# Kernel optimization log

Measured on AMD Instinct MI355X. Metric: run time of the kernel, lower is better.

## Reference

```python
import jax, jax.numpy as jnp
import numpy as np

N_CELLS = 4096          # rows of sparse x
N_INPUT_GENES = 20000   # cols of sparse x == len(input_gene_list)
N_PRETRAINED = 30000    # rows of embedding table
NUM_HID = 128
NNZ = 2097152           # ~512 expressed genes per cell


def setup_inputs() -> dict:
    key = jax.random.key(0)
    k_val, k_row, k_col, k_gidx, k_emb = jax.random.split(key, 5)
    x_values = jax.random.uniform(k_val, (NNZ,), dtype=jnp.float32)
    x_rows = jnp.sort(jax.random.randint(k_row, (NNZ,), 0, N_CELLS))
    x_cols = jax.random.randint(k_col, (NNZ,), 0, N_INPUT_GENES)
    gene_idx = jax.random.randint(k_gidx, (N_INPUT_GENES,), 0, N_PRETRAINED)
    # nn.Parameter(torch.randn(...) * 0.005)
    embs = jax.random.normal(k_emb, (N_PRETRAINED, NUM_HID), dtype=jnp.float32) * 0.005
    return {"x_values": x_values, "x_rows": x_rows, "x_cols": x_cols,
            "gene_idx": gene_idx, "embs": embs}


def reference(x_values, x_rows, x_cols, gene_idx, embs):
    # feat = F.embedding(gene_idx, embs)           -> [G_in, H]
    # out  = torch.sparse.mm(x, feat)              -> [N_cells, H]
    # Fused: gather per-nnz embedding rows, scale by value, segment-sum by cell.
    feat = embs[gene_idx]                                   # [G_in, H]
    contrib = x_values[:, None] * feat[x_cols]              # [NNZ, H]
    out = jax.ops.segment_sum(contrib, x_rows,
                              num_segments=N_CELLS,
                              indices_are_sorted=True)      # [N_cells, H]
    return out
```

## Files before the change

kernel.cpp:

```cpp
#include <hip/hip_runtime.h>

#define NNZ_TOT    2097152
#define N_CELLS    4096
#define N_GIN      20000
#define N_PRE      30000
#define NUM_HID    128

#define GA_OFF    0
#define GA_BYTES  ((size_t)NNZ_TOT * 4)
#define EBF_OFF   (GA_OFF + GA_BYTES)
#define EBF_BYTES ((size_t)N_PRE * NUM_HID * 2)
#define RP_OFF    (EBF_OFF + EBF_BYTES)
#define RP_BYTES  ((((size_t)(N_CELLS + 1) * 4) + 255) & ~(size_t)255)
#define WS_NEED   (RP_OFF + RP_BYTES)

__device__ __forceinline__ unsigned short f2bf(float f) {
    union { float f; unsigned u; } c; c.f = f;
    unsigned u = c.u;
    u += 0x7fffu + ((u >> 16) & 1u);
    return (unsigned short)(u >> 16);
}

#define NB_GA ((NNZ_TOT + 255) / 256)
#define NB_RP ((N_CELLS + 256) / 256)

__global__ __launch_bounds__(256) void precompute_kernel(
    const int* __restrict__ xc, const int* __restrict__ gidx,
    const int* __restrict__ xr, int* __restrict__ g_arr,
    int* __restrict__ rp)
{
    const int b = blockIdx.x;
    if (b < NB_GA) {
        const int i = b * 256 + threadIdx.x;
        if (i < NNZ_TOT) g_arr[i] = gidx[xc[i]];
    } else {
        const int r = (b - NB_GA) * 256 + threadIdx.x;
        if (r <= N_CELLS) {
            int lo = 0, hi = NNZ_TOT;
            while (lo < hi) {
                const int mid = (lo + hi) >> 1;
                if (xr[mid] < r) lo = mid + 1; else hi = mid;
            }
            rp[r] = lo;
        }
    }
}

__global__ __launch_bounds__(256) void convert_embs_kernel(
    const float* __restrict__ embs, unsigned short* __restrict__ ebf)
{
    const int i = blockIdx.x * blockDim.x + threadIdx.x;
    if (i * 4 < N_PRE * NUM_HID) {
        const float4 f = *reinterpret_cast<const float4*>(&embs[i * 4]);
        ushort4 o;
        o.x = f2bf(f.x); o.y = f2bf(f.y); o.z = f2bf(f.z); o.w = f2bf(f.w);
        *reinterpret_cast<ushort4*>(&ebf[i * 4]) = o;
    }
}

__device__ __forceinline__ void fma8(uint4 f, float vv, float4& a0, float4& a1) {
    a0.x = fmaf(vv, __uint_as_float(f.x << 16),         a0.x);
    a0.y = fmaf(vv, __uint_as_float(f.x & 0xffff0000u), a0.y);
    a0.z = fmaf(vv, __uint_as_float(f.y << 16),         a0.z);
    a0.w = fmaf(vv, __uint_as_float(f.y & 0xffff0000u), a0.w);
    a1.x = fmaf(vv, __uint_as_float(f.z << 16),         a1.x);
    a1.y = fmaf(vv, __uint_as_float(f.z & 0xffff0000u), a1.y);
    a1.z = fmaf(vv, __uint_as_float(f.w << 16),         a1.z);
    a1.w = fmaf(vv, __uint_as_float(f.w & 0xffff0000u), a1.w);
}

__global__ __launch_bounds__(256) void omics_row_kernel(
    const float*          __restrict__ xv,
    const int*            __restrict__ ga,
    const int*            __restrict__ rp,
    const unsigned short* __restrict__ ebf,
    float*                __restrict__ out)
{
    const int wave = (blockIdx.x * blockDim.x + threadIdx.x) >> 6;
    const int lane = threadIdx.x & 63;
    const int sub  = lane & 15;
    const int quad = lane >> 4;
    const int r    = __builtin_amdgcn_readfirstlane(wave);
    if (r >= N_CELLS) return;

    const int lo = rp[r];
    const int hi = rp[r + 1];
    const int h8 = sub * 8;

    float4 a0 = make_float4(0.f, 0.f, 0.f, 0.f);
    float4 a1 = make_float4(0.f, 0.f, 0.f, 0.f);
    float4 b0 = make_float4(0.f, 0.f, 0.f, 0.f);
    float4 b1 = make_float4(0.f, 0.f, 0.f, 0.f);

    int i = lo;
    for (; i + 32 <= hi; i += 32) {
        const int i0 = i + quad;
        const int g0 = ga[i0];      const float v0 = xv[i0];
        const int g1 = ga[i0 + 4];  const float v1 = xv[i0 + 4];
        const int g2 = ga[i0 + 8];  const float v2 = xv[i0 + 8];
        const int g3 = ga[i0 + 12]; const float v3 = xv[i0 + 12];
        const int g4 = ga[i0 + 16]; const float v4 = xv[i0 + 16];
        const int g5 = ga[i0 + 20]; const float v5 = xv[i0 + 20];
        const int g6 = ga[i0 + 24]; const float v6 = xv[i0 + 24];
        const int g7 = ga[i0 + 28]; const float v7 = xv[i0 + 28];

        const uint4 f0 = *reinterpret_cast<const uint4*>(&ebf[(long)g0 * NUM_HID + h8]);
        const uint4 f1 = *reinterpret_cast<const uint4*>(&ebf[(long)g1 * NUM_HID + h8]);
        const uint4 f2 = *reinterpret_cast<const uint4*>(&ebf[(long)g2 * NUM_HID + h8]);
        const uint4 f3 = *reinterpret_cast<const uint4*>(&ebf[(long)g3 * NUM_HID + h8]);
        const uint4 f4 = *reinterpret_cast<const uint4*>(&ebf[(long)g4 * NUM_HID + h8]);
        const uint4 f5 = *reinterpret_cast<const uint4*>(&ebf[(long)g5 * NUM_HID + h8]);
        const uint4 f6 = *reinterpret_cast<const uint4*>(&ebf[(long)g6 * NUM_HID + h8]);
        const uint4 f7 = *reinterpret_cast<const uint4*>(&ebf[(long)g7 * NUM_HID + h8]);

        fma8(f0, v0, a0, a1);
        fma8(f1, v1, b0, b1);
        fma8(f2, v2, a0, a1);
        fma8(f3, v3, b0, b1);
        fma8(f4, v4, a0, a1);
        fma8(f5, v5, b0, b1);
        fma8(f6, v6, a0, a1);
        fma8(f7, v7, b0, b1);
    }
    for (; i < hi; i += 4) {
        const int  idx = i + quad;
        const bool ok  = idx < hi;
        const int   gg = ga[ok ? idx : (hi - 1)];
        const float vv = ok ? xv[idx] : 0.f;
        const uint4 f  = *reinterpret_cast<const uint4*>(&ebf[(long)gg * NUM_HID + h8]);
        fma8(f, vv, a0, a1);
    }

    a0.x += b0.x; a0.y += b0.y; a0.z += b0.z; a0.w += b0.w;
    a1.x += b1.x; a1.y += b1.y; a1.z += b1.z; a1.w += b1.w;

    a0.x += __shfl_xor(a0.x, 16); a0.x += __shfl_xor(a0.x, 32);
    a0.y += __shfl_xor(a0.y, 16); a0.y += __shfl_xor(a0.y, 32);
    a0.z += __shfl_xor(a0.z, 16); a0.z += __shfl_xor(a0.z, 32);
    a0.w += __shfl_xor(a0.w, 16); a0.w += __shfl_xor(a0.w, 32);
    a1.x += __shfl_xor(a1.x, 16); a1.x += __shfl_xor(a1.x, 32);
    a1.y += __shfl_xor(a1.y, 16); a1.y += __shfl_xor(a1.y, 32);
    a1.z += __shfl_xor(a1.z, 16); a1.z += __shfl_xor(a1.z, 32);
    a1.w += __shfl_xor(a1.w, 16); a1.w += __shfl_xor(a1.w, 32);

    if (quad == 0) {
        float* o = &out[(long)r * NUM_HID + h8];
        *reinterpret_cast<float4*>(o)     = a0;
        *reinterpret_cast<float4*>(o + 4) = a1;
    }
}

__global__ __launch_bounds__(256) void omics_fp32_row_kernel(
    const float* __restrict__ xv, const int* __restrict__ xr,
    const int* __restrict__ xc, const int* __restrict__ gidx,
    const float* __restrict__ embs, float* __restrict__ out)
{
    const int wave = (blockIdx.x * blockDim.x + threadIdx.x) >> 6;
    const int lane = threadIdx.x & 63;
    if (wave >= N_CELLS) return;
    int lo = 0, hi = NNZ_TOT;
    while (lo < hi) { int m = (lo + hi) >> 1; if (xr[m] < wave) lo = m + 1; else hi = m; }
    int lo2 = lo, hi2 = NNZ_TOT;
    while (lo2 < hi2) { int m = (lo2 + hi2) >> 1; if (xr[m] < wave + 1) lo2 = m + 1; else hi2 = m; }
    const int h = lane * 2;
    float2 acc = make_float2(0.f, 0.f);
    for (int i = lo; i < lo2; ++i) {
        const float v = xv[i];
        const int   g = gidx[xc[i]];
        const float2 f = *reinterpret_cast<const float2*>(&embs[(long)g * NUM_HID + h]);
        acc.x = fmaf(v, f.x, acc.x);
        acc.y = fmaf(v, f.y, acc.y);
    }
    *reinterpret_cast<float2*>(&out[(long)wave * NUM_HID + h]) = acc;
}

extern "C" void kernel_launch(void* const* d_in, const int* in_sizes, int n_in,
                              void* d_out, int out_size, void* d_ws, size_t ws_size,
                              hipStream_t stream) {
    const float* xv   = (const float*)d_in[0];
    const int*   xr   = (const int*)  d_in[1];
    const int*   xc   = (const int*)  d_in[2];
    const int*   gidx = (const int*)  d_in[3];
    const float* embs = (const float*)d_in[4];
    float*       out  = (float*)d_out;

    if (ws_size >= WS_NEED) {
        int*            ga  = (int*)((char*)d_ws + GA_OFF);
        unsigned short* ebf = (unsigned short*)((char*)d_ws + EBF_OFF);
        int*            rp  = (int*)((char*)d_ws + RP_OFF);

        precompute_kernel<<<NB_GA + NB_RP, 256, 0, stream>>>(xc, gidx, xr, ga, rp);
        convert_embs_kernel<<<(N_PRE * NUM_HID / 4 + 255) / 256, 256, 0, stream>>>(embs, ebf);

        omics_row_kernel<<<(N_CELLS * 64) / 256, 256, 0, stream>>>(
            xv, ga, rp, ebf, out);
    } else {
        omics_fp32_row_kernel<<<(N_CELLS * 64) / 256, 256, 0, stream>>>(
            xv, xr, xc, gidx, embs, out);
    }
}
```

Baseline: 135.3 us.

## Split embedding table into column halves mapped to separate XCD groups

The bf16 embedding table is stored as two column halves, and each half of the output columns is computed by blocks whose index maps them to one group of four XCDs. The intent is to shrink the per-XCD L2 working set of gathered embedding rows so it fits in cache better. In exchange, each row's index and value streams are read twice, once per half, and those reads now use nontemporal loads and stores. The speedup depends on the round-robin block-to-XCD placement holding.

```diff
diff --git a/kernel.cpp b/kernel.cpp
--- a/kernel.cpp
+++ b/kernel.cpp
@@ -5,14 +5,18 @@
 #define N_GIN      20000
 #define N_PRE      30000
 #define NUM_HID    128
-
-#define GA_OFF    0
-#define GA_BYTES  ((size_t)NNZ_TOT * 4)
-#define EBF_OFF   (GA_OFF + GA_BYTES)
-#define EBF_BYTES ((size_t)N_PRE * NUM_HID * 2)
-#define RP_OFF    (EBF_OFF + EBF_BYTES)
-#define RP_BYTES  ((((size_t)(N_CELLS + 1) * 4) + 255) & ~(size_t)255)
-#define WS_NEED   (RP_OFF + RP_BYTES)
+#define HID_HALF   64
+
+#define GA_OFF     0
+#define GA_BYTES   ((size_t)NNZ_TOT * 4)
+#define EBFH_BYTES ((size_t)N_PRE * HID_HALF * 2)
+#define EBF0_OFF   (GA_OFF + GA_BYTES)
+#define EBF1_OFF   (EBF0_OFF + EBFH_BYTES)
+#define RP_OFF     (EBF1_OFF + EBFH_BYTES)
+#define RP_BYTES   ((((size_t)(N_CELLS + 1) * 4) + 255) & ~(size_t)255)
+#define WS_NEED    (RP_OFF + RP_BYTES)
+
+typedef float vfloat4 __attribute__((ext_vector_type(4)));
 
 __device__ __forceinline__ unsigned short f2bf(float f) {
     union { float f; unsigned u; } c; c.f = f;
@@ -47,14 +51,19 @@
 }
 
 __global__ __launch_bounds__(256) void convert_embs_kernel(
-    const float* __restrict__ embs, unsigned short* __restrict__ ebf)
+    const float* __restrict__ embs, unsigned short* __restrict__ ebf0,
+    unsigned short* __restrict__ ebf1)
 {
     const int i = blockIdx.x * blockDim.x + threadIdx.x;
-    if (i * 4 < N_PRE * NUM_HID) {
-        const float4 f = *reinterpret_cast<const float4*>(&embs[i * 4]);
+    const long idx = (long)i * 4;
+    if (idx < (long)N_PRE * NUM_HID) {
+        const float4 f = *reinterpret_cast<const float4*>(&embs[idx]);
         ushort4 o;
         o.x = f2bf(f.x); o.y = f2bf(f.y); o.z = f2bf(f.z); o.w = f2bf(f.w);
-        *reinterpret_cast<ushort4*>(&ebf[i * 4]) = o;
+        const int row = (int)(idx >> 7);
+        const int col = (int)(idx & 127);
+        unsigned short* __restrict__ dst = (col < HID_HALF) ? ebf0 : ebf1;
+        *reinterpret_cast<ushort4*>(&dst[row * HID_HALF + (col & 63)]) = o;
     }
 }
 
@@ -69,19 +78,25 @@
     a1.w = fmaf(vv, __uint_as_float(f.w & 0xffff0000u), a1.w);
 }
 
-__global__ __launch_bounds__(256) void omics_row_kernel(
+__global__ __launch_bounds__(256) void omics_half_kernel(
     const float*          __restrict__ xv,
     const int*            __restrict__ ga,
     const int*            __restrict__ rp,
-    const unsigned short* __restrict__ ebf,
+    const unsigned short* __restrict__ ebf0,
+    const unsigned short* __restrict__ ebf1,
     float*                __restrict__ out)
 {
-    const int wave = (blockIdx.x * blockDim.x + threadIdx.x) >> 6;
+    const int blk  = blockIdx.x;
+    const int xcd  = blk & 7;
+    const int half = xcd >> 2;
+    const int grp  = ((blk >> 3) << 2) | (xcd & 3);
+    const int wid  = threadIdx.x >> 6;
     const int lane = threadIdx.x & 63;
-    const int sub  = lane & 15;
-    const int quad = lane >> 4;
-    const int r    = __builtin_amdgcn_readfirstlane(wave);
-    if (r >= N_CELLS) return;
+    const int sub  = lane & 7;
+    const int oct  = lane >> 3;
+    const int r    = __builtin_amdgcn_readfirstlane((grp << 2) | wid);
+
+    const unsigned short* __restrict__ eb = half ? ebf1 : ebf0;
 
     const int lo = rp[r];
     const int hi = rp[r + 1];
@@ -93,25 +108,33 @@
     float4 b1 = make_float4(0.f, 0.f, 0.f, 0.f);
 
     int i = lo;
-    for (; i + 32 <= hi; i += 32) {
-        const int i0 = i + quad;
-        const int g0 = ga[i0];      const float v0 = xv[i0];
-        const int g1 = ga[i0 + 4];  const float v1 = xv[i0 + 4];
-        const int g2 = ga[i0 + 8];  const float v2 = xv[i0 + 8];
-        const int g3 = ga[i0 + 12]; const float v3 = xv[i0 + 12];
-        const int g4 = ga[i0 + 16]; const float v4 = xv[i0 + 16];
-        const int g5 = ga[i0 + 20]; const float v5 = xv[i0 + 20];
-        const int g6 = ga[i0 + 24]; const float v6 = xv[i0 + 24];
-        const int g7 = ga[i0 + 28]; const float v7 = xv[i0 + 28];
-
-        const uint4 f0 = *reinterpret_cast<const uint4*>(&ebf[(long)g0 * NUM_HID + h8]);
-        const uint4 f1 = *reinterpret_cast<const uint4*>(&ebf[(long)g1 * NUM_HID + h8]);
-        const uint4 f2 = *reinterpret_cast<const uint4*>(&ebf[(long)g2 * NUM_HID + h8]);
-        const uint4 f3 = *reinterpret_cast<const uint4*>(&ebf[(long)g3 * NUM_HID + h8]);
-        const uint4 f4 = *reinterpret_cast<const uint4*>(&ebf[(long)g4 * NUM_HID + h8]);
-        const uint4 f5 = *reinterpret_cast<const uint4*>(&ebf[(long)g5 * NUM_HID + h8]);
-        const uint4 f6 = *reinterpret_cast<const uint4*>(&ebf[(long)g6 * NUM_HID + h8]);
-        const uint4 f7 = *reinterpret_cast<const uint4*>(&ebf[(long)g7 * NUM_HID + h8]);
+    for (; i + 64 <= hi; i += 64) {
+        const int i0 = i + oct;
+        const int g0 = __builtin_nontemporal_load(ga + i0);
+        const int g1 = __builtin_nontemporal_load(ga + i0 + 8);
+        const int g2 = __builtin_nontemporal_load(ga + i0 + 16);
+        const int g3 = __builtin_nontemporal_load(ga + i0 + 24);
+        const int g4 = __builtin_nontemporal_load(ga + i0 + 32);
+        const int g5 = __builtin_nontemporal_load(ga + i0 + 40);
+        const int g6 = __builtin_nontemporal_load(ga + i0 + 48);
+        const int g7 = __builtin_nontemporal_load(ga + i0 + 56);
+        const float v0 = __builtin_nontemporal_load(xv + i0);
+        const float v1 = __builtin_nontemporal_load(xv + i0 + 8);
+        const float v2 = __builtin_nontemporal_load(xv + i0 + 16);
+        const float v3 = __builtin_nontemporal_load(xv + i0 + 24);
+        const float v4 = __builtin_nontemporal_load(xv + i0 + 32);
+        const float v5 = __builtin_nontemporal_load(xv + i0 + 40);
+        const float v6 = __builtin_nontemporal_load(xv + i0 + 48);
+        const float v7 = __builtin_nontemporal_load(xv + i0 + 56);
+
+        const uint4 f0 = *reinterpret_cast<const uint4*>(&eb[(long)g0 * HID_HALF + h8]);
+        const uint4 f1 = *reinterpret_cast<const uint4*>(&eb[(long)g1 * HID_HALF + h8]);
+        const uint4 f2 = *reinterpret_cast<const uint4*>(&eb[(long)g2 * HID_HALF + h8]);
+        const uint4 f3 = *reinterpret_cast<const uint4*>(&eb[(long)g3 * HID_HALF + h8]);
+        const uint4 f4 = *reinterpret_cast<const uint4*>(&eb[(long)g4 * HID_HALF + h8]);
+        const uint4 f5 = *reinterpret_cast<const uint4*>(&eb[(long)g5 * HID_HALF + h8]);
+        const uint4 f6 = *reinterpret_cast<const uint4*>(&eb[(long)g6 * HID_HALF + h8]);
+        const uint4 f7 = *reinterpret_cast<const uint4*>(&eb[(long)g7 * HID_HALF + h8]);
 
         fma8(f0, v0, a0, a1);
         fma8(f1, v1, b0, b1);
@@ -122,31 +145,33 @@
         fma8(f6, v6, a0, a1);
         fma8(f7, v7, b0, b1);
     }
-    for (; i < hi; i += 4) {
-        const int  idx = i + quad;
+    for (; i < hi; i += 8) {
+        const int  idx = i + oct;
         const bool ok  = idx < hi;
-        const int   gg = ga[ok ? idx : (hi - 1)];
+        const int   gg = ga[ok ? idx : lo];
         const float vv = ok ? xv[idx] : 0.f;
-        const uint4 f  = *reinterpret_cast<const uint4*>(&ebf[(long)gg * NUM_HID + h8]);
+        const uint4 f  = *reinterpret_cast<const uint4*>(&eb[(long)gg * HID_HALF + h8]);
         fma8(f, vv, a0, a1);
     }
 
     a0.x += b0.x; a0.y += b0.y; a0.z += b0.z; a0.w += b0.w;
     a1.x += b1.x; a1.y += b1.y; a1.z += b1.z; a1.w += b1.w;
 
-    a0.x += __shfl_xor(a0.x, 16); a0.x += __shfl_xor(a0.x, 32);
-    a0.y += __shfl_xor(a0.y, 16); a0.y += __shfl_xor(a0.y, 32);
-    a0.z += __shfl_xor(a0.z, 16); a0.z += __shfl_xor(a0.z, 32);
-    a0.w += __shfl_xor(a0.w, 16); a0.w += __shfl_xor(a0.w, 32);
-    a1.x += __shfl_xor(a1.x, 16); a1.x += __shfl_xor(a1.x, 32);
-    a1.y += __shfl_xor(a1.y, 16); a1.y += __shfl_xor(a1.y, 32);
-    a1.z += __shfl_xor(a1.z, 16); a1.z += __shfl_xor(a1.z, 32);
-    a1.w += __shfl_xor(a1.w, 16); a1.w += __shfl_xor(a1.w, 32);
-
-    if (quad == 0) {
-        float* o = &out[(long)r * NUM_HID + h8];
-        *reinterpret_cast<float4*>(o)     = a0;
-        *reinterpret_cast<float4*>(o + 4) = a1;
+    a0.x += __shfl_xor(a0.x, 8); a0.x += __shfl_xor(a0.x, 16); a0.x += __shfl_xor(a0.x, 32);
+    a0.y += __shfl_xor(a0.y, 8); a0.y += __shfl_xor(a0.y, 16); a0.y += __shfl_xor(a0.y, 32);
+    a0.z += __shfl_xor(a0.z, 8); a0.z += __shfl_xor(a0.z, 16); a0.z += __shfl_xor(a0.z, 32);
+    a0.w += __shfl_xor(a0.w, 8); a0.w += __shfl_xor(a0.w, 16); a0.w += __shfl_xor(a0.w, 32);
+    a1.x += __shfl_xor(a1.x, 8); a1.x += __shfl_xor(a1.x, 16); a1.x += __shfl_xor(a1.x, 32);
+    a1.y += __shfl_xor(a1.y, 8); a1.y += __shfl_xor(a1.y, 16); a1.y += __shfl_xor(a1.y, 32);
+    a1.z += __shfl_xor(a1.z, 8); a1.z += __shfl_xor(a1.z, 16); a1.z += __shfl_xor(a1.z, 32);
+    a1.w += __shfl_xor(a1.w, 8); a1.w += __shfl_xor(a1.w, 16); a1.w += __shfl_xor(a1.w, 32);
+
+    if (oct == 0) {
+        float* o = &out[(long)r * NUM_HID + half * HID_HALF + h8];
+        const vfloat4 s0 = { a0.x, a0.y, a0.z, a0.w };
+        const vfloat4 s1 = { a1.x, a1.y, a1.z, a1.w };
+        __builtin_nontemporal_store(s0, reinterpret_cast<vfloat4*>(o));
+        __builtin_nontemporal_store(s1, reinterpret_cast<vfloat4*>(o + 4));
     }
 }
 
@@ -185,15 +210,17 @@
     float*       out  = (float*)d_out;
 
     if (ws_size >= WS_NEED) {
-        int*            ga  = (int*)((char*)d_ws + GA_OFF);
-        unsigned short* ebf = (unsigned short*)((char*)d_ws + EBF_OFF);
-        int*            rp  = (int*)((char*)d_ws + RP_OFF);
+        int*            ga   = (int*)((char*)d_ws + GA_OFF);
+        unsigned short* ebf0 = (unsigned short*)((char*)d_ws + EBF0_OFF);
+        unsigned short* ebf1 = (unsigned short*)((char*)d_ws + EBF1_OFF);
+        int*            rp   = (int*)((char*)d_ws + RP_OFF);
 
         precompute_kernel<<<NB_GA + NB_RP, 256, 0, stream>>>(xc, gidx, xr, ga, rp);
-        convert_embs_kernel<<<(N_PRE * NUM_HID / 4 + 255) / 256, 256, 0, stream>>>(embs, ebf);
-
-        omics_row_kernel<<<(N_CELLS * 64) / 256, 256, 0, stream>>>(
-            xv, ga, rp, ebf, out);
+        convert_embs_kernel<<<(N_PRE * NUM_HID / 4 + 255) / 256, 256, 0, stream>>>(
+            embs, ebf0, ebf1);
+
+        omics_half_kernel<<<(N_CELLS / 4) * 2, 256, 0, stream>>>(
+            xv, ga, rp, ebf0, ebf1, out);
     } else {
         omics_fp32_row_kernel<<<(N_CELLS * 64) / 256, 256, 0, stream>>>(
             xv, xr, xc, gidx, embs, out);
```

Result: slower. 144.0 us (+6.4%).

## Quantize embedding table to 8-bit with global absmax scale for gather

Applied to the files above, without the earlier changes.

Replaces the bf16 copy of the embedding table with an unsigned 8-bit quantized copy. The scale comes from a global absmax found by extra blocks in the precompute kernel. The row kernel gathers 16 bytes per lane covering 16 hidden values, so eight lanes cover a row and each wave processes eight nonzeros per step. The +128 offset is removed at the end using the sum of the values. This halves gather traffic from the table, but precision drops to about 7 bits relative to the max, which risks failing accuracy tolerance, and it adds a memset and a reduction pass.

```diff
diff --git a/kernel.cpp b/kernel.cpp
--- a/kernel.cpp
+++ b/kernel.cpp
@@ -8,32 +8,29 @@
 
 #define GA_OFF    0
 #define GA_BYTES  ((size_t)NNZ_TOT * 4)
-#define EBF_OFF   (GA_OFF + GA_BYTES)
-#define EBF_BYTES ((size_t)N_PRE * NUM_HID * 2)
-#define RP_OFF    (EBF_OFF + EBF_BYTES)
+#define E8_OFF    (GA_OFF + GA_BYTES)
+#define E8_BYTES  ((size_t)N_PRE * NUM_HID)
+#define RP_OFF    (E8_OFF + E8_BYTES)
 #define RP_BYTES  ((((size_t)(N_CELLS + 1) * 4) + 255) & ~(size_t)255)
-#define WS_NEED   (RP_OFF + RP_BYTES)
-
-__device__ __forceinline__ unsigned short f2bf(float f) {
-    union { float f; unsigned u; } c; c.f = f;
-    unsigned u = c.u;
-    u += 0x7fffu + ((u >> 16) & 1u);
-    return (unsigned short)(u >> 16);
-}
+#define SC_OFF    (RP_OFF + RP_BYTES)
+#define SC_BYTES  256
+#define WS_NEED   (SC_OFF + SC_BYTES)
 
 #define NB_GA ((NNZ_TOT + 255) / 256)
 #define NB_RP ((N_CELLS + 256) / 256)
+#define NB_MX 512
 
 __global__ __launch_bounds__(256) void precompute_kernel(
     const int* __restrict__ xc, const int* __restrict__ gidx,
-    const int* __restrict__ xr, int* __restrict__ g_arr,
-    int* __restrict__ rp)
+    const int* __restrict__ xr, const float* __restrict__ embs,
+    int* __restrict__ g_arr, int* __restrict__ rp,
+    unsigned int* __restrict__ sc)
 {
     const int b = blockIdx.x;
     if (b < NB_GA) {
         const int i = b * 256 + threadIdx.x;
         if (i < NNZ_TOT) g_arr[i] = gidx[xc[i]];
-    } else {
+    } else if (b < NB_GA + NB_RP) {
         const int r = (b - NB_GA) * 256 + threadIdx.x;
         if (r <= N_CELLS) {
             int lo = 0, hi = NNZ_TOT;
@@ -43,110 +40,158 @@
             }
             rp[r] = lo;
         }
-    }
-}
-
-__global__ __launch_bounds__(256) void convert_embs_kernel(
-    const float* __restrict__ embs, unsigned short* __restrict__ ebf)
+    } else {
+        const int t = (b - NB_GA - NB_RP) * 256 + (int)threadIdx.x;
+        const float4* __restrict__ e4 = reinterpret_cast<const float4*>(embs);
+        float m = 0.f;
+        for (int j = t; j < N_PRE * NUM_HID / 4; j += NB_MX * 256) {
+            const float4 f = e4[j];
+            m = fmaxf(m, fmaxf(fmaxf(fabsf(f.x), fabsf(f.y)),
+                               fmaxf(fabsf(f.z), fabsf(f.w))));
+        }
+        for (int d = 1; d < 64; d <<= 1) m = fmaxf(m, __shfl_xor(m, d));
+        if ((threadIdx.x & 63) == 0) atomicMax(sc, __float_as_uint(m));
+    }
+}
+
+__global__ __launch_bounds__(256) void convert_embs8_kernel(
+    const float* __restrict__ embs, const unsigned int* __restrict__ sc,
+    unsigned int* __restrict__ e8)
 {
     const int i = blockIdx.x * blockDim.x + threadIdx.x;
-    if (i * 4 < N_PRE * NUM_HID) {
-        const float4 f = *reinterpret_cast<const float4*>(&embs[i * 4]);
-        ushort4 o;
-        o.x = f2bf(f.x); o.y = f2bf(f.y); o.z = f2bf(f.z); o.w = f2bf(f.w);
-        *reinterpret_cast<ushort4*>(&ebf[i * 4]) = o;
-    }
-}
-
-__device__ __forceinline__ void fma8(uint4 f, float vv, float4& a0, float4& a1) {
-    a0.x = fmaf(vv, __uint_as_float(f.x << 16),         a0.x);
-    a0.y = fmaf(vv, __uint_as_float(f.x & 0xffff0000u), a0.y);
-    a0.z = fmaf(vv, __uint_as_float(f.y << 16),         a0.z);
-    a0.w = fmaf(vv, __uint_as_float(f.y & 0xffff0000u), a0.w);
-    a1.x = fmaf(vv, __uint_as_float(f.z << 16),         a1.x);
-    a1.y = fmaf(vv, __uint_as_float(f.z & 0xffff0000u), a1.y);
-    a1.z = fmaf(vv, __uint_as_float(f.w << 16),         a1.z);
-    a1.w = fmaf(vv, __uint_as_float(f.w & 0xffff0000u), a1.w);
-}
-
-__global__ __launch_bounds__(256) void omics_row_kernel(
-    const float*          __restrict__ xv,
-    const int*            __restrict__ ga,
-    const int*            __restrict__ rp,
-    const unsigned short* __restrict__ ebf,
-    float*                __restrict__ out)
+    const long idx = (long)i * 4;
+    if (idx < (long)N_PRE * NUM_HID) {
+        const float maxabs = __uint_as_float(*sc);
+        const float s = (maxabs > 0.f) ? 127.0f / maxabs : 0.f;
+        const float4 f = *reinterpret_cast<const float4*>(&embs[idx]);
+        int b0 = (int)rintf(f.x * s) + 128;
+        int b1 = (int)rintf(f.y * s) + 128;
+        int b2 = (int)rintf(f.z * s) + 128;
+        int b3 = (int)rintf(f.w * s) + 128;
+        b0 = min(max(b0, 0), 255); b1 = min(max(b1, 0), 255);
+        b2 = min(max(b2, 0), 255); b3 = min(max(b3, 0), 255);
+        e8[i] = (unsigned)b0 | ((unsigned)b1 << 8) |
+                ((unsigned)b2 << 16) | ((unsigned)b3 << 24);
+    }
+}
+
+#define U2F0(w) ((float)((w) & 0xffu))
+#define U2F1(w) ((float)(((w) >> 8)  & 0xffu))
+#define U2F2(w) ((float)(((w) >> 16) & 0xffu))
+#define U2F3(w) ((float)(((w) >> 24) & 0xffu))
+
+__device__ __forceinline__ void fma16i(uint4 f, float vv,
+                                       float4& a0, float4& a1,
+                                       float4& a2, float4& a3, float& S) {
+    a0.x = fmaf(vv, U2F0(f.x), a0.x);
+    a0.y = fmaf(vv, U2F1(f.x), a0.y);
+    a0.z = fmaf(vv, U2F2(f.x), a0.z);
+    a0.w = fmaf(vv, U2F3(f.x), a0.w);
+    a1.x = fmaf(vv, U2F0(f.y), a1.x);
+    a1.y = fmaf(vv, U2F1(f.y), a1.y);
+    a1.z = fmaf(vv, U2F2(f.y), a1.z);
+    a1.w = fmaf(vv, U2F3(f.y), a1.w);
+    a2.x = fmaf(vv, U2F0(f.z), a2.x);
+    a2.y = fmaf(vv, U2F1(f.z), a2.y);
+    a2.z = fmaf(vv, U2F2(f.z), a2.z);
+    a2.w = fmaf(vv, U2F3(f.z), a2.w);
+    a3.x = fmaf(vv, U2F0(f.w), a3.x);
+    a3.y = fmaf(vv, U2F1(f.w), a3.y);
+    a3.z = fmaf(vv, U2F2(f.w), a3.z);
+    a3.w = fmaf(vv, U2F3(f.w), a3.w);
+    S += vv;
+}
+
+__global__ __launch_bounds__(256) void omics_row8_kernel(
+    const float*        __restrict__ xv,
+    const int*          __restrict__ ga,
+    const int*          __restrict__ rp,
+    const unsigned int* __restrict__ e8,
+    const unsigned int* __restrict__ sc,
+    float*              __restrict__ out)
 {
     const int wave = (blockIdx.x * blockDim.x + threadIdx.x) >> 6;
     const int lane = threadIdx.x & 63;
-    const int sub  = lane & 15;
-    const int quad = lane >> 4;
+    const int sub  = lane & 7;
+    const int oct  = lane >> 3;
     const int r    = __builtin_amdgcn_readfirstlane(wave);
     if (r >= N_CELLS) return;
 
+    const uint4* __restrict__ ebq = reinterpret_cast<const uint4*>(e8);
+
     const int lo = rp[r];
     const int hi = rp[r + 1];
-    const int h8 = sub * 8;
-
-    float4 a0 = make_float4(0.f, 0.f, 0.f, 0.f);
-    float4 a1 = make_float4(0.f, 0.f, 0.f, 0.f);
-    float4 b0 = make_float4(0.f, 0.f, 0.f, 0.f);
-    float4 b1 = make_float4(0.f, 0.f, 0.f, 0.f);
+
+    float4 a0 = make_float4(0.f,0.f,0.f,0.f), a1 = a0, a2 = a0, a3 = a0;
+    float4 b0 = a0, b1 = a0, b2 = a0, b3 = a0;
+    float Sa = 0.f, Sb = 0.f;
 
     int i = lo;
-    for (; i + 32 <= hi; i += 32) {
-        const int i0 = i + quad;
+    for (; i + 64 <= hi; i += 64) {
+        const int i0 = i + oct;
         const int g0 = ga[i0];      const float v0 = xv[i0];
-        const int g1 = ga[i0 + 4];  const float v1 = xv[i0 + 4];
-        const int g2 = ga[i0 + 8];  const float v2 = xv[i0 + 8];
-        const int g3 = ga[i0 + 12]; const float v3 = xv[i0 + 12];
-        const int g4 = ga[i0 + 16]; const float v4 = xv[i0 + 16];
-        const int g5 = ga[i0 + 20]; const float v5 = xv[i0 + 20];
-        const int g6 = ga[i0 + 24]; const float v6 = xv[i0 + 24];
-        const int g7 = ga[i0 + 28]; const float v7 = xv[i0 + 28];
-
-        const uint4 f0 = *reinterpret_cast<const uint4*>(&ebf[(long)g0 * NUM_HID + h8]);
-        const uint4 f1 = *reinterpret_cast<const uint4*>(&ebf[(long)g1 * NUM_HID + h8]);
-        const uint4 f2 = *reinterpret_cast<const uint4*>(&ebf[(long)g2 * NUM_HID + h8]);
-        const uint4 f3 = *reinterpret_cast<const uint4*>(&ebf[(long)g3 * NUM_HID + h8]);
-        const uint4 f4 = *reinterpret_cast<const uint4*>(&ebf[(long)g4 * NUM_HID + h8]);
-        const uint4 f5 = *reinterpret_cast<const uint4*>(&ebf[(long)g5 * NUM_HID + h8]);
-        const uint4 f6 = *reinterpret_cast<const uint4*>(&ebf[(long)g6 * NUM_HID + h8]);
-        const uint4 f7 = *reinterpret_cast<const uint4*>(&ebf[(long)g7 * NUM_HID + h8]);
-
-        fma8(f0, v0, a0, a1);
-        fma8(f1, v1, b0, b1);
-        fma8(f2, v2, a0, a1);
-        fma8(f3, v3, b0, b1);
-        fma8(f4, v4, a0, a1);
-        fma8(f5, v5, b0, b1);
-        fma8(f6, v6, a0, a1);
-        fma8(f7, v7, b0, b1);
-    }
-    for (; i < hi; i += 4) {
-        const int  idx = i + quad;
+        const int g1 = ga[i0 + 8];  const float v1 = xv[i0 + 8];
+        const int g2 = ga[i0 + 16]; const float v2 = xv[i0 + 16];
+        const int g3 = ga[i0 + 24]; const float v3 = xv[i0 + 24];
+        const int g4 = ga[i0 + 32]; const float v4 = xv[i0 + 32];
+        const int g5 = ga[i0 + 40]; const float v5 = xv[i0 + 40];
+        const int g6 = ga[i0 + 48]; const float v6 = xv[i0 + 48];
+        const int g7 = ga[i0 + 56]; const float v7 = xv[i0 + 56];
+
+        const uint4 f0 = ebq[(long)g0 * 8 + sub];
+        const uint4 f1 = ebq[(long)g1 * 8 + sub];
+        const uint4 f2 = ebq[(long)g2 * 8 + sub];
+        const uint4 f3 = ebq[(long)g3 * 8 + sub];
+        const uint4 f4 = ebq[(long)g4 * 8 + sub];
+        const uint4 f5 = ebq[(long)g5 * 8 + sub];
+        const uint4 f6 = ebq[(long)g6 * 8 + sub];
+        const uint4 f7 = ebq[(long)g7 * 8 + sub];
+
+        fma16i(f0, v0, a0, a1, a2, a3, Sa);
+        fma16i(f1, v1, b0, b1, b2, b3, Sb);
+        fma16i(f2, v2, a0, a1, a2, a3, Sa);
+        fma16i(f3, v3, b0, b1, b2, b3, Sb);
+        fma16i(f4, v4, a0, a1, a2, a3, Sa);
+        fma16i(f5, v5, b0, b1, b2, b3, Sb);
+        fma16i(f6, v6, a0, a1, a2, a3, Sa);
+        fma16i(f7, v7, b0, b1, b2, b3, Sb);
+    }
+    for (; i < hi; i += 8) {
+        const int  idx = i + oct;
         const bool ok  = idx < hi;
-        const int   gg = ga[ok ? idx : (hi - 1)];
+        const int   gg = ga[ok ? idx : lo];
         const float vv = ok ? xv[idx] : 0.f;
-        const uint4 f  = *reinterpret_cast<const uint4*>(&ebf[(long)gg * NUM_HID + h8]);
-        fma8(f, vv, a0, a1);
+        const uint4 f  = ebq[(long)gg * 8 + sub];
+        fma16i(f, vv, a0, a1, a2, a3, Sa);
     }
 
     a0.x += b0.x; a0.y += b0.y; a0.z += b0.z; a0.w += b0.w;
     a1.x += b1.x; a1.y += b1.y; a1.z += b1.z; a1.w += b1.w;
-
-    a0.x += __shfl_xor(a0.x, 16); a0.x += __shfl_xor(a0.x, 32);
-    a0.y += __shfl_xor(a0.y, 16); a0.y += __shfl_xor(a0.y, 32);
-    a0.z += __shfl_xor(a0.z, 16); a0.z += __shfl_xor(a0.z, 32);
-    a0.w += __shfl_xor(a0.w, 16); a0.w += __shfl_xor(a0.w, 32);
-    a1.x += __shfl_xor(a1.x, 16); a1.x += __shfl_xor(a1.x, 32);
-    a1.y += __shfl_xor(a1.y, 16); a1.y += __shfl_xor(a1.y, 32);
-    a1.z += __shfl_xor(a1.z, 16); a1.z += __shfl_xor(a1.z, 32);
-    a1.w += __shfl_xor(a1.w, 16); a1.w += __shfl_xor(a1.w, 32);
-
-    if (quad == 0) {
-        float* o = &out[(long)r * NUM_HID + h8];
-        *reinterpret_cast<float4*>(o)     = a0;
-        *reinterpret_cast<float4*>(o + 4) = a1;
+    a2.x += b2.x; a2.y += b2.y; a2.z += b2.z; a2.w += b2.w;
+    a3.x += b3.x; a3.y += b3.y; a3.z += b3.z; a3.w += b3.w;
+    Sa += Sb;
+
+    #define RED(c) c += __shfl_xor(c, 8); c += __shfl_xor(c, 16); c += __shfl_xor(c, 32)
+    RED(a0.x); RED(a0.y); RED(a0.z); RED(a0.w);
+    RED(a1.x); RED(a1.y); RED(a1.z); RED(a1.w);
+    RED(a2.x); RED(a2.y); RED(a2.z); RED(a2.w);
+    RED(a3.x); RED(a3.y); RED(a3.z); RED(a3.w);
+    RED(Sa);
+    #undef RED
+
+    if (oct == 0) {
+        const float maxabs = __uint_as_float(*sc);
+        const float sdec   = (maxabs > 0.f) ? maxabs / 127.0f : 0.f;
+        const float c      = 128.0f * Sa;
+        float* o = &out[(long)r * NUM_HID + sub * 16];
+        *reinterpret_cast<float4*>(o)      = make_float4(
+            sdec*(a0.x-c), sdec*(a0.y-c), sdec*(a0.z-c), sdec*(a0.w-c));
+        *reinterpret_cast<float4*>(o + 4)  = make_float4(
+            sdec*(a1.x-c), sdec*(a1.y-c), sdec*(a1.z-c), sdec*(a1.w-c));
+        *reinterpret_cast<float4*>(o + 8)  = make_float4(
+            sdec*(a2.x-c), sdec*(a2.y-c), sdec*(a2.z-c), sdec*(a2.w-c));
+        *reinterpret_cast<float4*>(o + 12) = make_float4(
+            sdec*(a3.x-c), sdec*(a3.y-c), sdec*(a3.z-c), sdec*(a3.w-c));
     }
 }
 
@@ -185,15 +230,20 @@
     float*       out  = (float*)d_out;
 
     if (ws_size >= WS_NEED) {
-        int*            ga  = (int*)((char*)d_ws + GA_OFF);
-        unsigned short* ebf = (unsigned short*)((char*)d_ws + EBF_OFF);
-        int*            rp  = (int*)((char*)d_ws + RP_OFF);
-
-        precompute_kernel<<<NB_GA + NB_RP, 256, 0, stream>>>(xc, gidx, xr, ga, rp);
-        convert_embs_kernel<<<(N_PRE * NUM_HID / 4 + 255) / 256, 256, 0, stream>>>(embs, ebf);
-
-        omics_row_kernel<<<(N_CELLS * 64) / 256, 256, 0, stream>>>(
-            xv, ga, rp, ebf, out);
+        int*          ga = (int*)((char*)d_ws + GA_OFF);
+        unsigned int* e8 = (unsigned int*)((char*)d_ws + E8_OFF);
+        int*          rp = (int*)((char*)d_ws + RP_OFF);
+        unsigned int* sc = (unsigned int*)((char*)d_ws + SC_OFF);
+
+        (void)hipMemsetAsync(sc, 0, 4, stream);
+
+        precompute_kernel<<<NB_GA + NB_RP + NB_MX, 256, 0, stream>>>(
+            xc, gidx, xr, embs, ga, rp, sc);
+        convert_embs8_kernel<<<(N_PRE * NUM_HID / 4 + 255) / 256, 256, 0, stream>>>(
+            embs, sc, e8);
+
+        omics_row8_kernel<<<(N_CELLS * 64) / 256, 256, 0, stream>>>(
+            xv, ga, rp, e8, sc, out);
     } else {
         omics_fp32_row_kernel<<<(N_CELLS * 64) / 256, 256, 0, stream>>>(
             xv, xr, xc, gidx, embs, out);
```

After: 141.9 us. +4.8%, slower.
